# Performance work log

Measured on AMD Instinct MI355X. Metric: run time of the kernel, lower is better.

The kernel has to match this reference:

```python
import jax, jax.numpy as jnp
import numpy as np
from jax import lax

B, Hs, Ws = 2, 256, 256
DIM = 256        # query channels (c)
DIM_BAK = 256    # key/value channels (c2)
HEADS = 8
WIN = 8
HEAD_DIM = DIM // HEADS
SCALE = HEAD_DIM ** -0.5


def window_partition(x, ws):
    # x: [B, H, W, C] -> [B*nH*nW, ws, ws, C]
    b, h, w, c = x.shape
    x = x.reshape(b, h // ws, ws, w // ws, ws, c)
    return x.transpose(0, 1, 3, 2, 4, 5).reshape(-1, ws, ws, c)


def window_reverse(windows, ws, h, w):
    # windows: [B*nH*nW, ws, ws, C] -> [B, H, W, C]
    b = windows.shape[0] // ((h // ws) * (w // ws))
    x = windows.reshape(b, h // ws, w // ws, ws, ws, -1)
    return x.transpose(0, 1, 3, 2, 4, 5).reshape(b, h, w, -1)


def setup_inputs() -> dict:
    key = jax.random.key(0)
    ks = jax.random.split(key, 9)
    s = 0.02
    return {
        "query_feature": jax.random.normal(ks[0], (B, DIM, Hs, Ws), jnp.float32),
        "key_value_feature": jax.random.normal(ks[1], (B, DIM_BAK, Hs, Ws), jnp.float32),
        # depthwise 3x3 conv on kv (groups=DIM_BAK, bias=False): OIHW with I=1
        "w_dw": jax.random.normal(ks[2], (DIM_BAK, 1, 3, 3), jnp.float32) * s,
        # to_q: Linear(dim -> dim), stored [in, out]
        "wq": jax.random.normal(ks[3], (DIM, DIM), jnp.float32) * s,
        "bq": jax.random.normal(ks[4], (DIM,), jnp.float32) * s,
        # to_kv: Linear(dim_bak -> 2*dim)
        "wkv": jax.random.normal(ks[5], (DIM_BAK, 2 * DIM), jnp.float32) * s,
        "bkv": jax.random.normal(ks[6], (2 * DIM,), jnp.float32) * s,
        # project_out: Linear(dim -> dim)
        "w_proj": jax.random.normal(ks[7], (DIM, DIM), jnp.float32) * s,
        "b_proj": jax.random.normal(ks[8], (DIM,), jnp.float32) * s,
    }


def reference(query_feature, key_value_feature, w_dw, wq, bq, wkv, bkv, w_proj, b_proj):
    b, c, h, w = query_feature.shape
    c2 = key_value_feature.shape[1]

    # depthwise 3x3 conv on key/value feature (padding=1, stride=1)
    kv = lax.conv_general_dilated(
        key_value_feature, w_dw,
        window_strides=(1, 1), padding="SAME",
        feature_group_count=c2,
        dimension_numbers=("NCHW", "OIHW", "NCHW"))

    # NCHW -> NHWC, partition into non-overlapping windows
    qw = window_partition(query_feature.transpose(0, 2, 3, 1), WIN)  # [B_, ws, ws, c]
    kvw = window_partition(kv.transpose(0, 2, 3, 1), WIN)            # [B_, ws, ws, c2]
    B_ = qw.shape[0]
    N = WIN * WIN
    qw = qw.reshape(B_, N, c)
    kvw = kvw.reshape(B_, N, c2)

    # projections -> multi-head [B_, heads, N, head_dim]
    q = (qw @ wq + bq).reshape(B_, N, HEADS, HEAD_DIM).transpose(0, 2, 1, 3) * SCALE
    kv_proj = (kvw @ wkv + bkv).reshape(B_, N, 2, HEADS, HEAD_DIM)
    k = kv_proj[:, :, 0].transpose(0, 2, 1, 3)
    v = kv_proj[:, :, 1].transpose(0, 2, 1, 3)

    # windowed cross-attention
    attn = jax.nn.softmax(jnp.einsum("bhnd,bhmd->bhnm", q, k), axis=-1)
    out = jnp.einsum("bhnm,bhmd->bhnd", attn, v)
    out = out.transpose(0, 2, 1, 3).reshape(B_, N, c)
    out = out @ w_proj + b_proj

    # reverse windows, back to NCHW
    out = window_reverse(out.reshape(B_, WIN, WIN, c), WIN, h, w)
    return out.transpose(0, 3, 1, 2)
```

## Files before the change

### kernel.cpp

```cpp
#include <hip/hip_runtime.h>
#include <hip/hip_bf16.h>
#include <cstdint>
#include <cstddef>

typedef __hip_bfloat16 bf16;
typedef short bf16x8 __attribute__((ext_vector_type(8)));
typedef float f32x4 __attribute__((ext_vector_type(4)));

#define MFMA(a, b, c) __builtin_amdgcn_mfma_f32_16x16x32_bf16((a), (b), (c), 0, 0, 0)

__global__ __launch_bounds__(256) void transpose_k(const float* __restrict__ src,
                                                   bf16* __restrict__ dst, int K, int N) {
  int idx = blockIdx.x * 256 + threadIdx.x;
  if (idx >= K * N) return;
  int n = idx / K, k = idx - n * K;
  dst[idx] = __float2bfloat16(src[k * N + n]);
}

__global__ __launch_bounds__(256) void conv_gather_k(const float* __restrict__ kvf,
                                                     const float* __restrict__ wdw,
                                                     bf16* __restrict__ kvw,
                                                     int wid_base, int nw) {
  int bid = blockIdx.x;
  int sw = (bid & 7) * (nw >> 3) + (bid >> 3);
  int wid = wid_base + sw;
  int b = wid >> 10, rem = wid & 1023, wh = rem >> 5, ww = rem & 31;
  int h0 = wh * 8, w0 = ww * 8;
  int c = threadIdx.x;
  const float* src = kvf + ((size_t)(b * 256 + c) << 16) + w0;
  float wr[9];
#pragma unroll
  for (int q = 0; q < 9; ++q) wr[q] = wdw[c * 9 + q];
  const bool wlo = (w0 > 0), whi = (w0 < 248);

  float rows[3][10];
  auto load_row = [&](int gh, float* r) {
    if (gh >= 0 && gh < 256) {
      const float* rp = src + gh * 256;
      r[0] = wlo ? rp[-1] : 0.f;
      f32x4 a4 = *(const f32x4*)&rp[0];
      f32x4 b4 = *(const f32x4*)&rp[4];
#pragma unroll
      for (int e = 0; e < 4; ++e) {
        r[1 + e] = a4[e];
        r[5 + e] = b4[e];
      }
      r[9] = whi ? rp[8] : 0.f;
    } else {
#pragma unroll
      for (int e = 0; e < 10; ++e) r[e] = 0.f;
    }
  };

  load_row(h0 - 1, rows[0]);
  load_row(h0, rows[1]);
#pragma unroll
  for (int i = 0; i < 8; ++i) {
    load_row(h0 + i + 1, rows[(i + 2) % 3]);
#pragma unroll
    for (int j = 0; j < 8; ++j) {
      float acc = 0.f;
#pragma unroll
      for (int di = 0; di < 3; ++di) {
        const float* rp = rows[(i + di) % 3];
        acc = __builtin_fmaf(wr[di * 3 + 0], rp[j], acc);
        acc = __builtin_fmaf(wr[di * 3 + 1], rp[j + 1], acc);
        acc = __builtin_fmaf(wr[di * 3 + 2], rp[j + 2], acc);
      }
      kvw[((size_t)(sw * 64 + i * 8 + j) << 8) + c] = __float2bfloat16(acc);
    }
  }
}

__global__ __launch_bounds__(256) void kv_gemm_k(const bf16* __restrict__ kvw,
                                                 const bf16* __restrict__ wkvT,
                                                 const float* __restrict__ bkv,
                                                 bf16* __restrict__ k_s,
                                                 bf16* __restrict__ vT_s,
                                                 int wid_base, int nw) {
  __shared__ __align__(16) bf16 X[64 * 264];
  int bid = blockIdx.x;
  int sw = (bid & 7) * (nw >> 3) + (bid >> 3);
  int tid = threadIdx.x;
  {
    int t = tid >> 2, cb = (tid & 3) * 64;
    const bf16* src = &kvw[((size_t)(sw * 64 + t) << 8) + cb];
    bf16* dst = &X[t * 264 + cb];
    for (int i = 0; i < 8; ++i) *(bf16x8*)&dst[i * 8] = *(const bf16x8*)&src[i * 8];
  }
  __syncthreads();
  int wave = tid >> 6, lane = tid & 63, quad = lane >> 4, l16 = lane & 15;
  int n0 = wave * 128;
  f32x4 zero4 = {0.f, 0.f, 0.f, 0.f};
  f32x4 acc[4][8];
  for (int mt = 0; mt < 4; ++mt)
    for (int nt = 0; nt < 8; ++nt) acc[mt][nt] = zero4;
  for (int k0 = 0; k0 < 256; k0 += 32) {
    bf16x8 a[4], bb[8];
    for (int mt = 0; mt < 4; ++mt)
      a[mt] = *(const bf16x8*)&X[(mt * 16 + l16) * 264 + k0 + quad * 8];
    for (int nt = 0; nt < 8; ++nt)
      bb[nt] = *(const bf16x8*)&wkvT[(size_t)(n0 + nt * 16 + l16) * 256 + k0 + quad * 8];
    for (int mt = 0; mt < 4; ++mt)
      for (int nt = 0; nt < 8; ++nt) acc[mt][nt] = MFMA(a[mt], bb[nt], acc[mt][nt]);
  }
  __syncthreads();
  for (int nt = 0; nt < 8; ++nt) {
    int n = n0 + nt * 16 + l16;
    float bias = bkv[n];
    if (n < 256) {
      for (int mt = 0; mt < 4; ++mt) {
        int mb = mt * 16 + quad * 4;
        for (int r = 0; r < 4; ++r)
          k_s[((size_t)(sw * 64 + mb + r) << 8) + n] =
              __float2bfloat16(acc[mt][nt][r] + bias);
      }
    } else {
      int d = n - 256;
      for (int mt = 0; mt < 4; ++mt) {
        int mb = mt * 16 + quad * 4;
        for (int r = 0; r < 4; ++r)
          X[(mb + r) * 264 + d] = __float2bfloat16(acc[mt][nt][r] + bias);
      }
    }
  }
  __syncthreads();
  {
    int t = tid & 63, d0 = tid >> 6;
    for (int d = d0; d < 256; d += 4)
      vT_s[((size_t)(sw * 256 + d) << 6) + t] = X[t * 264 + d];
  }
}

__global__ __launch_bounds__(256) void q_gemm_k(const float* __restrict__ qf,
                                                const bf16* __restrict__ wqT,
                                                const float* __restrict__ bq,
                                                bf16* __restrict__ q_s,
                                                int wid_base, int nw) {
  __shared__ __align__(16) bf16 X[64 * 264];
  int bid = blockIdx.x;
  int sw = (bid & 7) * (nw >> 3) + (bid >> 3);
  int wid = wid_base + sw;
  int b = wid >> 10, rem = wid & 1023, wh = rem >> 5, ww = rem & 31;
  int h0 = wh * 8, w0 = ww * 8;
  int tid = threadIdx.x;
  {
    int c = tid;
    const float* src = qf + ((size_t)(b * 256 + c) << 16) + (size_t)h0 * 256 + w0;
#pragma unroll
    for (int i = 0; i < 8; ++i) {
      f32x4 a4 = *(const f32x4*)&src[i * 256];
      f32x4 b4 = *(const f32x4*)&src[i * 256 + 4];
#pragma unroll
      for (int e = 0; e < 4; ++e) {
        X[(i * 8 + e) * 264 + c] = __float2bfloat16(a4[e]);
        X[(i * 8 + 4 + e) * 264 + c] = __float2bfloat16(b4[e]);
      }
    }
  }
  __syncthreads();
  int wave = tid >> 6, lane = tid & 63, quad = lane >> 4, l16 = lane & 15;
  int n0 = wave * 64;
  f32x4 zero4 = {0.f, 0.f, 0.f, 0.f};
  f32x4 acc[4][4];
  for (int mt = 0; mt < 4; ++mt)
    for (int nt = 0; nt < 4; ++nt) acc[mt][nt] = zero4;
  for (int k0 = 0; k0 < 256; k0 += 32) {
    bf16x8 a[4], bb[4];
    for (int mt = 0; mt < 4; ++mt)
      a[mt] = *(const bf16x8*)&X[(mt * 16 + l16) * 264 + k0 + quad * 8];
    for (int nt = 0; nt < 4; ++nt)
      bb[nt] = *(const bf16x8*)&wqT[(size_t)(n0 + nt * 16 + l16) * 256 + k0 + quad * 8];
    for (int mt = 0; mt < 4; ++mt)
      for (int nt = 0; nt < 4; ++nt) acc[mt][nt] = MFMA(a[mt], bb[nt], acc[mt][nt]);
  }
  const float scale = 0.1767766952966369f;
  for (int nt = 0; nt < 4; ++nt) {
    int n = n0 + nt * 16 + l16;
    float bias = bq[n];
    for (int mt = 0; mt < 4; ++mt) {
      int mb = mt * 16 + quad * 4;
      for (int r = 0; r < 4; ++r)
        q_s[((size_t)(sw * 64 + mb + r) << 8) + n] =
            __float2bfloat16((acc[mt][nt][r] + bias) * scale);
    }
  }
}

__global__ __launch_bounds__(256) void attn_k(const bf16* __restrict__ q_s,
                                              const bf16* k_s,
                                              const bf16* __restrict__ vT_s,
                                              bf16* a_out,
                                              int wid_base, int nw) {
  __shared__ __align__(16) bf16 P[4 * 64 * 72];
  int bid = blockIdx.x;
  int sw = (bid & 7) * (nw >> 3) + (bid >> 3);
  int tid = threadIdx.x, wave = tid >> 6, lane = tid & 63, quad = lane >> 4, l16 = lane & 15;
  const bf16* qw = q_s + ((size_t)sw << 14);
  const bf16* kw = k_s + ((size_t)sw << 14);
  const bf16* vw = vT_s + ((size_t)sw << 14);
  bf16* ow = a_out + ((size_t)sw << 14);
  bf16* Pw = P + wave * 64 * 72;
  f32x4 zero4 = {0.f, 0.f, 0.f, 0.f};
  for (int hi = 0; hi < 2; ++hi) {
    int co = (wave + hi * 4) * 32;
    f32x4 s[4][4];
    for (int mt = 0; mt < 4; ++mt)
      for (int nt = 0; nt < 4; ++nt) s[mt][nt] = zero4;
    {
      bf16x8 a[4], bb[4];
      for (int mt = 0; mt < 4; ++mt)
        a[mt] = *(const bf16x8*)&qw[(size_t)(mt * 16 + l16) * 256 + co + quad * 8];
      for (int nt = 0; nt < 4; ++nt)
        bb[nt] = *(const bf16x8*)&kw[(size_t)(nt * 16 + l16) * 256 + co + quad * 8];
      for (int mt = 0; mt < 4; ++mt)
        for (int nt = 0; nt < 4; ++nt) s[mt][nt] = MFMA(a[mt], bb[nt], s[mt][nt]);
    }
    float rsum[4][4];
    for (int mt = 0; mt < 4; ++mt) {
      for (int r = 0; r < 4; ++r) {
        float m = s[mt][0][r];
        for (int nt = 1; nt < 4; ++nt) m = fmaxf(m, s[mt][nt][r]);
        m = fmaxf(m, __shfl_xor(m, 1, 64));
        m = fmaxf(m, __shfl_xor(m, 2, 64));
        m = fmaxf(m, __shfl_xor(m, 4, 64));
        m = fmaxf(m, __shfl_xor(m, 8, 64));
        float sum = 0.f;
        for (int nt = 0; nt < 4; ++nt) {
          float e = __expf(s[mt][nt][r] - m);
          s[mt][nt][r] = e;
          sum += e;
        }
        sum += __shfl_xor(sum, 1, 64);
        sum += __shfl_xor(sum, 2, 64);
        sum += __shfl_xor(sum, 4, 64);
        sum += __shfl_xor(sum, 8, 64);
        rsum[mt][r] = sum;
      }
    }
    for (int mt = 0; mt < 4; ++mt)
      for (int nt = 0; nt < 4; ++nt)
        for (int r = 0; r < 4; ++r)
          Pw[(mt * 16 + quad * 4 + r) * 72 + nt * 16 + l16] =
              __float2bfloat16(s[mt][nt][r]);
    __syncthreads();
    f32x4 o[4][2];
    for (int mt = 0; mt < 4; ++mt)
      for (int nt = 0; nt < 2; ++nt) o[mt][nt] = zero4;
    for (int kk = 0; kk < 64; kk += 32) {
      bf16x8 pa[4], vb[2];
      for (int mt = 0; mt < 4; ++mt)
        pa[mt] = *(const bf16x8*)&Pw[(mt * 16 + l16) * 72 + kk + quad * 8];
      for (int nt = 0; nt < 2; ++nt)
        vb[nt] = *(const bf16x8*)&vw[(size_t)(co + nt * 16 + l16) * 64 + kk + quad * 8];
      for (int mt = 0; mt < 4; ++mt)
        for (int nt = 0; nt < 2; ++nt) o[mt][nt] = MFMA(pa[mt], vb[nt], o[mt][nt]);
    }
    for (int mt = 0; mt < 4; ++mt) {
      int mb = mt * 16 + quad * 4;
      for (int nt = 0; nt < 2; ++nt)
        for (int r = 0; r < 4; ++r)
          ow[((size_t)(mb + r) << 8) + co + nt * 16 + l16] =
              __float2bfloat16(o[mt][nt][r] / rsum[mt][r]);
    }
    __syncthreads();
  }
}

__global__ __launch_bounds__(256) void oproj_k(const bf16* __restrict__ a_out,
                                               const bf16* __restrict__ wpT,
                                               const float* __restrict__ bp,
                                               float* __restrict__ out,
                                               int wid_base, int nw) {
  int bid = blockIdx.x;
  int sw = (bid & 7) * (nw >> 3) + (bid >> 3);
  int wid = wid_base + sw;
  int b = wid >> 10, rem = wid & 1023, wh = rem >> 5, ww = rem & 31;
  int h0 = wh * 8, w0 = ww * 8;
  int tid = threadIdx.x, wave = tid >> 6, lane = tid & 63, quad = lane >> 4, l16 = lane & 15;
  const bf16* aw = a_out + ((size_t)sw << 14);
  int n0 = wave * 64;
  f32x4 zero4 = {0.f, 0.f, 0.f, 0.f};
  f32x4 acc[4][4];
  for (int mt = 0; mt < 4; ++mt)
    for (int nt = 0; nt < 4; ++nt) acc[mt][nt] = zero4;
  for (int k0 = 0; k0 < 256; k0 += 32) {
    bf16x8 a[4], bb[4];
    for (int mt = 0; mt < 4; ++mt)
      a[mt] = *(const bf16x8*)&aw[(size_t)(mt * 16 + l16) * 256 + k0 + quad * 8];
    for (int nt = 0; nt < 4; ++nt)
      bb[nt] = *(const bf16x8*)&wpT[(size_t)(n0 + nt * 16 + l16) * 256 + k0 + quad * 8];
    for (int mt = 0; mt < 4; ++mt)
      for (int nt = 0; nt < 4; ++nt) acc[mt][nt] = MFMA(a[mt], bb[nt], acc[mt][nt]);
  }
  for (int nt = 0; nt < 4; ++nt) {
    int n = n0 + nt * 16 + l16;
    float bias = bp[n];
    float* chan = out + ((size_t)(b * 256 + n) << 16);
    for (int mt = 0; mt < 4; ++mt) {
      int row_i = mt * 2 + (quad >> 1);
      int j0 = (quad & 1) * 4;
      f32x4 v4;
      for (int r = 0; r < 4; ++r) v4[r] = acc[mt][nt][r] + bias;
      *(f32x4*)&chan[(size_t)(h0 + row_i) * 256 + w0 + j0] = v4;
    }
  }
}

extern "C" void kernel_launch(void* const* d_in, const int* in_sizes, int n_in,
                              void* d_out, int out_size, void* d_ws, size_t ws_size,
                              hipStream_t stream) {
  const float* qf  = (const float*)d_in[0];
  const float* kvf = (const float*)d_in[1];
  const float* wdw = (const float*)d_in[2];
  const float* wq  = (const float*)d_in[3];
  const float* bq  = (const float*)d_in[4];
  const float* wkv = (const float*)d_in[5];
  const float* bkv = (const float*)d_in[6];
  const float* wp  = (const float*)d_in[7];
  const float* bp  = (const float*)d_in[8];
  float* out = (float*)d_out;

  bf16* wqT  = (bf16*)d_ws;
  bf16* wkvT = wqT + 256 * 256;
  bf16* wpT  = wkvT + 256 * 512;
  bf16* bufs = wpT + 256 * 256;
  size_t wbytes = (size_t)(256 * 256 + 256 * 512 + 256 * 256) * sizeof(bf16);
  size_t remb = ws_size > wbytes ? ws_size - wbytes : 0;
  int passes = 1;
  while (passes < 32 && (size_t)3 * (2048 / passes) * 64 * 256 * 2 > remb) passes <<= 1;
  int nw = 2048 / passes;
  size_t sz = (size_t)nw * 64 * 256;
  bf16* R0 = bufs;
  bf16* R1 = R0 + sz;
  bf16* R2 = R1 + sz;

  transpose_k<<<256, 256, 0, stream>>>(wq, wqT, 256, 256);
  transpose_k<<<512, 256, 0, stream>>>(wkv, wkvT, 256, 512);
  transpose_k<<<256, 256, 0, stream>>>(wp, wpT, 256, 256);

  for (int p = 0; p < passes; ++p) {
    int wb = p * nw;
    conv_gather_k<<<nw, 256, 0, stream>>>(kvf, wdw, R0, wb, nw);
    kv_gemm_k<<<nw, 256, 0, stream>>>(R0, wkvT, bkv, R1, R2, wb, nw);
    q_gemm_k<<<nw, 256, 0, stream>>>(qf, wqT, bq, R0, wb, nw);
    attn_k<<<nw, 256, 0, stream>>>(R0, R1, R2, R1, wb, nw);
    oproj_k<<<nw, 256, 0, stream>>>(R1, wpT, bp, out, wb, nw);
  }
}
```

Baseline: 667.4 us.

## Pre-transpose NCHW inputs to bf16 NHWC tiles before conv and q projection

Adds shared-memory transpose kernels that turn the fp32 NCHW query and key/value features into channel-last bf16 buffers. The query is written directly in window order, and the key/value feature goes into a row-range buffer with halo rows, which the depthwise conv then reads channel-contiguously. The kv GEMM now writes V transposed straight from registers by swapping the MFMA operands in the V waves, which removes the LDS round trip and two barriers. This replaces strided per-channel fp32 reads with coalesced accesses, at the cost of extra kernel launches, an extra intermediate write and read, and rounding the conv input to bf16.

```diff
diff --git a/kernel.cpp b/kernel.cpp
--- a/kernel.cpp
+++ b/kernel.cpp
@@ -17,17 +17,73 @@
   dst[idx] = __float2bfloat16(src[k * N + n]);
 }
 
-__global__ __launch_bounds__(256) void conv_gather_k(const float* __restrict__ kvf,
-                                                     const float* __restrict__ wdw,
-                                                     bf16* __restrict__ kvw,
-                                                     int wid_base, int nw) {
+__global__ __launch_bounds__(256) void t_winq_k(const float* __restrict__ src,
+                                                bf16* __restrict__ dst,
+                                                int hw0, int swoff) {
+  __shared__ bf16 T[64][66];
+  int tile = blockIdx.x;
+  int c0 = (tile & 3) << 6;
+  int hwb = hw0 + ((tile >> 2) << 6);
+  int tid = threadIdx.x;
+  {
+    int hwl = tid & 63, cb = tid >> 6;
+    const float* s = src + (size_t)(c0 + cb) * 65536 + hwb + hwl;
+#pragma unroll
+    for (int i = 0; i < 16; ++i)
+      T[cb + i * 4][hwl] = __float2bfloat16(s[(size_t)i * 4 * 65536]);
+  }
+  __syncthreads();
+  {
+    int cl = tid & 63, hb = tid >> 6;
+#pragma unroll
+    for (int j = 0; j < 16; ++j) {
+      int hwl = hb + j * 4;
+      int hw = hwb + hwl;
+      int h = hw >> 8, w = hw & 255;
+      int sw = swoff + ((h >> 3) << 5) + (w >> 3);
+      int t = ((h & 7) << 3) + (w & 7);
+      dst[((size_t)(sw * 64 + t) << 8) + c0 + cl] = T[cl][hwl];
+    }
+  }
+}
+
+__global__ __launch_bounds__(256) void t_nhwc_k(const float* __restrict__ src,
+                                                bf16* __restrict__ dst, int hw0) {
+  __shared__ bf16 T[64][66];
+  int tile = blockIdx.x;
+  int c0 = (tile & 3) << 6;
+  int hwoff = (tile >> 2) << 6;
+  int tid = threadIdx.x;
+  {
+    int hwl = tid & 63, cb = tid >> 6;
+    const float* s = src + (size_t)(c0 + cb) * 65536 + hw0 + hwoff + hwl;
+#pragma unroll
+    for (int i = 0; i < 16; ++i)
+      T[cb + i * 4][hwl] = __float2bfloat16(s[(size_t)i * 4 * 65536]);
+  }
+  __syncthreads();
+  {
+    int cl = tid & 63, hb = tid >> 6;
+#pragma unroll
+    for (int j = 0; j < 16; ++j) {
+      int hwl = hb + j * 4;
+      dst[((size_t)(hwoff + hwl) << 8) + c0 + cl] = T[cl][hwl];
+    }
+  }
+}
+
+__global__ __launch_bounds__(256) void conv_k(const bf16* __restrict__ kvbC,
+                                              const float* __restrict__ wdw,
+                                              bf16* __restrict__ kvw,
+                                              int wid_base, int cw, int psw0,
+                                              int h_start) {
   int bid = blockIdx.x;
-  int sw = (bid & 7) * (nw >> 3) + (bid >> 3);
-  int wid = wid_base + sw;
-  int b = wid >> 10, rem = wid & 1023, wh = rem >> 5, ww = rem & 31;
+  int swc = (bid & 7) * (cw >> 3) + (bid >> 3);
+  int wid = wid_base + swc;
+  int rem = wid & 1023, wh = rem >> 5, ww = rem & 31;
   int h0 = wh * 8, w0 = ww * 8;
+  int osw = psw0 + swc;
   int c = threadIdx.x;
-  const float* src = kvf + ((size_t)(b * 256 + c) << 16) + w0;
   float wr[9];
 #pragma unroll
   for (int q = 0; q < 9; ++q) wr[q] = wdw[c * 9 + q];
@@ -36,16 +92,11 @@
   float rows[3][10];
   auto load_row = [&](int gh, float* r) {
     if (gh >= 0 && gh < 256) {
-      const float* rp = src + gh * 256;
-      r[0] = wlo ? rp[-1] : 0.f;
-      f32x4 a4 = *(const f32x4*)&rp[0];
-      f32x4 b4 = *(const f32x4*)&rp[4];
-#pragma unroll
-      for (int e = 0; e < 4; ++e) {
-        r[1 + e] = a4[e];
-        r[5 + e] = b4[e];
-      }
-      r[9] = whi ? rp[8] : 0.f;
+      const bf16* rp = kvbC + ((size_t)((gh - h_start) * 256 + w0) << 8) + c;
+      r[0] = wlo ? __bfloat162float(rp[-256]) : 0.f;
+#pragma unroll
+      for (int s = 1; s <= 8; ++s) r[s] = __bfloat162float(rp[(s - 1) * 256]);
+      r[9] = whi ? __bfloat162float(rp[8 * 256]) : 0.f;
     } else {
 #pragma unroll
       for (int e = 0; e < 10; ++e) r[e] = 0.f;
@@ -67,7 +118,7 @@
         acc = __builtin_fmaf(wr[di * 3 + 1], rp[j + 1], acc);
         acc = __builtin_fmaf(wr[di * 3 + 2], rp[j + 2], acc);
       }
-      kvw[((size_t)(sw * 64 + i * 8 + j) << 8) + c] = __float2bfloat16(acc);
+      kvw[((size_t)(osw * 64 + i * 8 + j) << 8) + c] = __float2bfloat16(acc);
     }
   }
 }
@@ -76,8 +127,7 @@
                                                  const bf16* __restrict__ wkvT,
                                                  const float* __restrict__ bkv,
                                                  bf16* __restrict__ k_s,
-                                                 bf16* __restrict__ vT_s,
-                                                 int wid_base, int nw) {
+                                                 bf16* __restrict__ vT_s, int nw) {
   __shared__ __align__(16) bf16 X[64 * 264];
   int bid = blockIdx.x;
   int sw = (bid & 7) * (nw >> 3) + (bid >> 3);
@@ -95,68 +145,65 @@
   f32x4 acc[4][8];
   for (int mt = 0; mt < 4; ++mt)
     for (int nt = 0; nt < 8; ++nt) acc[mt][nt] = zero4;
-  for (int k0 = 0; k0 < 256; k0 += 32) {
-    bf16x8 a[4], bb[8];
-    for (int mt = 0; mt < 4; ++mt)
-      a[mt] = *(const bf16x8*)&X[(mt * 16 + l16) * 264 + k0 + quad * 8];
-    for (int nt = 0; nt < 8; ++nt)
-      bb[nt] = *(const bf16x8*)&wkvT[(size_t)(n0 + nt * 16 + l16) * 256 + k0 + quad * 8];
-    for (int mt = 0; mt < 4; ++mt)
-      for (int nt = 0; nt < 8; ++nt) acc[mt][nt] = MFMA(a[mt], bb[nt], acc[mt][nt]);
-  }
-  __syncthreads();
-  for (int nt = 0; nt < 8; ++nt) {
-    int n = n0 + nt * 16 + l16;
-    float bias = bkv[n];
-    if (n < 256) {
+  if (wave < 2) {
+    for (int k0 = 0; k0 < 256; k0 += 32) {
+      bf16x8 a[4], bb[8];
+      for (int mt = 0; mt < 4; ++mt)
+        a[mt] = *(const bf16x8*)&X[(mt * 16 + l16) * 264 + k0 + quad * 8];
+      for (int nt = 0; nt < 8; ++nt)
+        bb[nt] = *(const bf16x8*)&wkvT[(size_t)(n0 + nt * 16 + l16) * 256 + k0 + quad * 8];
+      for (int mt = 0; mt < 4; ++mt)
+        for (int nt = 0; nt < 8; ++nt) acc[mt][nt] = MFMA(a[mt], bb[nt], acc[mt][nt]);
+    }
+  } else {
+    for (int k0 = 0; k0 < 256; k0 += 32) {
+      bf16x8 a[4], bb[8];
+      for (int mt = 0; mt < 4; ++mt)
+        a[mt] = *(const bf16x8*)&X[(mt * 16 + l16) * 264 + k0 + quad * 8];
+      for (int nt = 0; nt < 8; ++nt)
+        bb[nt] = *(const bf16x8*)&wkvT[(size_t)(n0 + nt * 16 + l16) * 256 + k0 + quad * 8];
+      for (int mt = 0; mt < 4; ++mt)
+        for (int nt = 0; nt < 8; ++nt) acc[mt][nt] = MFMA(bb[nt], a[mt], acc[mt][nt]);
+    }
+  }
+  if (wave < 2) {
+    for (int nt = 0; nt < 8; ++nt) {
+      int n = n0 + nt * 16 + l16;
+      float bias = bkv[n];
       for (int mt = 0; mt < 4; ++mt) {
         int mb = mt * 16 + quad * 4;
         for (int r = 0; r < 4; ++r)
           k_s[((size_t)(sw * 64 + mb + r) << 8) + n] =
               __float2bfloat16(acc[mt][nt][r] + bias);
       }
-    } else {
-      int d = n - 256;
-      for (int mt = 0; mt < 4; ++mt) {
-        int mb = mt * 16 + quad * 4;
-        for (int r = 0; r < 4; ++r)
-          X[(mb + r) * 264 + d] = __float2bfloat16(acc[mt][nt][r] + bias);
+    }
+  } else {
+    int base = n0 - 256;
+    for (int nt = 0; nt < 8; ++nt) {
+      for (int r = 0; r < 4; ++r) {
+        int vd = base + nt * 16 + quad * 4 + r;
+        float bias = bkv[256 + vd];
+        for (int mt = 0; mt < 4; ++mt)
+          vT_s[((size_t)(sw * 256 + vd) << 6) + mt * 16 + l16] =
+              __float2bfloat16(acc[mt][nt][r] + bias);
       }
     }
   }
-  __syncthreads();
-  {
-    int t = tid & 63, d0 = tid >> 6;
-    for (int d = d0; d < 256; d += 4)
-      vT_s[((size_t)(sw * 256 + d) << 6) + t] = X[t * 264 + d];
-  }
-}
-
-__global__ __launch_bounds__(256) void q_gemm_k(const float* __restrict__ qf,
+}
+
+__global__ __launch_bounds__(256) void q_gemm_k(const bf16* __restrict__ qwM,
                                                 const bf16* __restrict__ wqT,
                                                 const float* __restrict__ bq,
-                                                bf16* __restrict__ q_s,
-                                                int wid_base, int nw) {
+                                                bf16* __restrict__ q_s, int nw) {
   __shared__ __align__(16) bf16 X[64 * 264];
   int bid = blockIdx.x;
   int sw = (bid & 7) * (nw >> 3) + (bid >> 3);
-  int wid = wid_base + sw;
-  int b = wid >> 10, rem = wid & 1023, wh = rem >> 5, ww = rem & 31;
-  int h0 = wh * 8, w0 = ww * 8;
   int tid = threadIdx.x;
   {
-    int c = tid;
-    const float* src = qf + ((size_t)(b * 256 + c) << 16) + (size_t)h0 * 256 + w0;
-#pragma unroll
-    for (int i = 0; i < 8; ++i) {
-      f32x4 a4 = *(const f32x4*)&src[i * 256];
-      f32x4 b4 = *(const f32x4*)&src[i * 256 + 4];
-#pragma unroll
-      for (int e = 0; e < 4; ++e) {
-        X[(i * 8 + e) * 264 + c] = __float2bfloat16(a4[e]);
-        X[(i * 8 + 4 + e) * 264 + c] = __float2bfloat16(b4[e]);
-      }
-    }
+    int t = tid >> 2, cb = (tid & 3) * 64;
+    const bf16* src = &qwM[((size_t)(sw * 64 + t) << 8) + cb];
+    bf16* dst = &X[t * 264 + cb];
+    for (int i = 0; i < 8; ++i) *(bf16x8*)&dst[i * 8] = *(const bf16x8*)&src[i * 8];
   }
   __syncthreads();
   int wave = tid >> 6, lane = tid & 63, quad = lane >> 4, l16 = lane & 15;
@@ -190,8 +237,7 @@
 __global__ __launch_bounds__(256) void attn_k(const bf16* __restrict__ q_s,
                                               const bf16* k_s,
                                               const bf16* __restrict__ vT_s,
-                                              bf16* a_out,
-                                              int wid_base, int nw) {
+                                              bf16* a_out, int nw) {
   __shared__ __align__(16) bf16 P[4 * 64 * 72];
   int bid = blockIdx.x;
   int sw = (bid & 7) * (nw >> 3) + (bid >> 3);
@@ -325,26 +371,52 @@
   bf16* wkvT = wqT + 256 * 256;
   bf16* wpT  = wkvT + 256 * 512;
   bf16* bufs = wpT + 256 * 256;
-  size_t wbytes = (size_t)(256 * 256 + 256 * 512 + 256 * 256) * sizeof(bf16);
-  size_t remb = ws_size > wbytes ? ws_size - wbytes : 0;
+  const size_t welems = 65536 + 131072 + 65536;
+
   int passes = 1;
-  while (passes < 32 && (size_t)3 * (2048 / passes) * 64 * 256 * 2 > remb) passes <<= 1;
+  while (passes < 32) {
+    size_t nw_ = 2048 / passes;
+    size_t elems = welems + 5 * nw_ * 16384 + 4 * 65536;
+    if (elems * 2 <= ws_size) break;
+    passes <<= 1;
+  }
   int nw = 2048 / passes;
-  size_t sz = (size_t)nw * 64 * 256;
-  bf16* R0 = bufs;
-  bf16* R1 = R0 + sz;
-  bf16* R2 = R1 + sz;
+  size_t sz = (size_t)nw * 16384;
+  bf16* qwM = bufs;
+  bf16* kvb = qwM + sz;
+  bf16* R0  = kvb + sz + 4 * 65536;
+  bf16* R1  = R0 + sz;
+  bf16* R2  = R1 + sz;
 
   transpose_k<<<256, 256, 0, stream>>>(wq, wqT, 256, 256);
   transpose_k<<<512, 256, 0, stream>>>(wkv, wkvT, 256, 512);
   transpose_k<<<256, 256, 0, stream>>>(wp, wpT, 256, 256);
 
   for (int p = 0; p < passes; ++p) {
-    int wb = p * nw;
-    conv_gather_k<<<nw, 256, 0, stream>>>(kvf, wdw, R0, wb, nw);
-    kv_gemm_k<<<nw, 256, 0, stream>>>(R0, wkvT, bkv, R1, R2, wb, nw);
-    q_gemm_k<<<nw, 256, 0, stream>>>(qf, wqT, bq, R0, wb, nw);
-    attn_k<<<nw, 256, 0, stream>>>(R0, R1, R2, R1, wb, nw);
-    oproj_k<<<nw, 256, 0, stream>>>(R1, wpT, bp, out, wb, nw);
-  }
-}
+    int wbP = p * nw;
+    int nchunks = (nw > 1024) ? 2 : 1;
+    int cw = nw / nchunks;
+    for (int ch = 0; ch < nchunks; ++ch) {
+      int wbC = wbP + ch * cw;
+      int b = wbC >> 10;
+      int h0 = ((wbC & 1023) >> 5) * 8;
+      int nh = (cw >> 5) * 8;
+      int psw0 = ch * cw;
+      const float* qsrc = qf + ((size_t)b << 24);
+      const float* ksrc = kvf + ((size_t)b << 24);
+      t_winq_k<<<cw * 4, 256, 0, stream>>>(qsrc, qwM, h0 * 256, b * 1024 - wbP);
+      int gh_lo = h0 > 0 ? h0 - 1 : 0;
+      int gh_hi = (h0 + nh + 1 < 256) ? h0 + nh + 1 : 256;
+      int rows = gh_hi - gh_lo;
+      int h_start = h0 - 1;
+      bf16* kvbC = kvb + (size_t)ch * (size_t)(nh + 2) * 65536;
+      bf16* tdst = kvbC + (size_t)(gh_lo - h_start) * 65536;
+      t_nhwc_k<<<rows * 16, 256, 0, stream>>>(ksrc, tdst, gh_lo * 256);
+      conv_k<<<cw, 256, 0, stream>>>(kvbC, wdw, R0, wbC, cw, psw0, h_start);
+    }
+    kv_gemm_k<<<nw, 256, 0, stream>>>(R0, wkvT, bkv, R1, R2, nw);
+    q_gemm_k<<<nw, 256, 0, stream>>>(qwM, wqT, bq, R0, nw);
+    attn_k<<<nw, 256, 0, stream>>>(R0, R1, R2, R1, nw);
+    oproj_k<<<nw, 256, 0, stream>>>(R1, wpT, bp, out, wbP, nw);
+  }
+}
```

Measured after the change: 720.1 us. +7.9%, slower.
